# Kernel tuning notes

Measured on AMD Instinct MI355X. Metric: run time of the kernel, lower is better.

The kernel has to match this reference:

```python
import jax, jax.numpy as jnp
import numpy as np

N, H, I, B = 128, 128, 2, 8192

def _gru(x, h, Wih, Whh, bih, bhh):
    # torch.nn.GRUCell semantics; gates ordered (r, z, n)
    gi = x @ Wih.T + bih              # [B, 3H]
    gh = h @ Whh.T + bhh              # [B, 3H]
    ir, iz, ic = jnp.split(gi, 3, axis=1)
    hr, hz, hc = jnp.split(gh, 3, axis=1)
    r = jax.nn.sigmoid(ir + hr)
    z = jax.nn.sigmoid(iz + hz)
    n = jnp.tanh(ic + r * hc)
    return (1.0 - z) * n + z * h

def setup_inputs() -> dict:
    key = jax.random.key(0)
    ks = jax.random.split(key, 13)
    s = 0.1  # ~1/sqrt(H) init scale
    return {
        "inputs": jax.random.uniform(ks[0], (B, I), jnp.float32),
        "Wih0": jax.random.normal(ks[1], (N, 3 * H, I), jnp.float32) * s,
        "Whh0": jax.random.normal(ks[2], (N, 3 * H, H), jnp.float32) * s,
        "bih0": jax.random.normal(ks[3], (N, 3 * H), jnp.float32) * s,
        "bhh0": jax.random.normal(ks[4], (N, 3 * H), jnp.float32) * s,
        "Wih1": jax.random.normal(ks[5], (N, 3 * H, H), jnp.float32) * s,
        "Whh1": jax.random.normal(ks[6], (N, 3 * H, H), jnp.float32) * s,
        "bih1": jax.random.normal(ks[7], (N, 3 * H), jnp.float32) * s,
        "bhh1": jax.random.normal(ks[8], (N, 3 * H), jnp.float32) * s,
        "W1": jax.random.normal(ks[9], (N, H, H), jnp.float32) * s,
        "b1": jax.random.normal(ks[10], (N, H), jnp.float32) * s,
        "W2": jax.random.normal(ks[11], (N, I, H), jnp.float32) * s,
        "b2": jax.random.normal(ks[12], (N, I), jnp.float32) * s,
    }

def reference(inputs, Wih0, Whh0, bih0, bhh0, Wih1, Whh1, bih1, bhh1, W1, b1, W2, b2):
    batch = inputs.shape[0]
    h0 = jnp.zeros((batch, H), inputs.dtype)
    sample_keys = jax.random.split(jax.random.key(42), N)

    def step(carry, xs):
        inp, h1, h2 = carry
        (wih0, whh0, bi0, bh0, wih1, whh1, bi1, bh1, w1, bb1, w2, bb2, k) = xs
        h1 = _gru(inp, h1, wih0, whh0, bi0, bh0)
        h2 = _gru(h1, h2, wih1, whh1, bi1, bh1)
        s = jnp.cos(h2) + 1e-10
        hdn = jax.nn.relu(s @ w1.T + bb1)
        p = jax.nn.softmax(hdn @ w2.T + bb2, axis=1) + 1e-10  # probs + eps, as in torch
        sample = jax.lax.stop_gradient(jax.random.categorical(k, jnp.log(p)))
        nxt = jax.nn.one_hot(sample, I, dtype=p.dtype)
        return (nxt, h1, h2), p

    xs = (Wih0, Whh0, bih0, bhh0, Wih1, Whh1, bih1, bhh1, W1, b1, W2, b2, sample_keys)
    _, probs = jax.lax.scan(step, (inputs, h0, h0), xs)  # probs: [N, B, I]
    return jnp.transpose(probs, (1, 0, 2))  # [B, N, I]
```

## Files before the change

### kernel.cpp

```cpp
#include <hip/hip_runtime.h>
#include <cstdint>


namespace {

constexpr int NSTEPS = 128;
constexpr int HDIM = 128;
constexpr int G3H = 384;

constexpr int BTM = 32;
constexpr int THM = 512;
constexpr int S0P = 385;
constexpr int S1P = 513;

constexpr int BT = 16;
constexpr int THREADS = 256;
constexpr int HP = 132;
constexpr int SP = 516;

typedef _Float16 half8 __attribute__((ext_vector_type(8)));
typedef float f32x4 __attribute__((ext_vector_type(4)));

constexpr float LO_SCALE = 4096.0f;
constexpr float LO_INV = 2.44140625e-4f;
constexpr float F16_MIN_NORM = 6.104e-5f;
constexpr float LOG2E = 1.4426950408889634f;
constexpr float INV2PI = 0.15915494309189535f;

__device__ __forceinline__ void split_f16(float x, _Float16& a1, _Float16& a2s) {
  _Float16 h = (fabsf(x) < F16_MIN_NORM) ? (_Float16)0.0f : (_Float16)x;
  a1 = h;
  a2s = (_Float16)((x - (float)h) * LO_SCALE);
}

__device__ __forceinline__ void tf2x32(uint32_t k0, uint32_t k1,
                                       uint32_t x0, uint32_t x1,
                                       uint32_t& o0, uint32_t& o1) {
  const uint32_t ks2 = k0 ^ k1 ^ 0x1BD11BDAu;
  uint32_t v0 = x0 + k0;
  uint32_t v1 = x1 + k1;
  const uint32_t ks[3] = {k0, k1, ks2};
  const uint32_t rotA[4] = {13u, 15u, 26u, 6u};
  const uint32_t rotB[4] = {17u, 29u, 16u, 24u};
#pragma unroll
  for (int i = 0; i < 5; ++i) {
#pragma unroll
    for (int j = 0; j < 4; ++j) {
      const uint32_t r = (i & 1) ? rotB[j] : rotA[j];
      v0 += v1;
      v1 = (v1 << r) | (v1 >> (32u - r));
      v1 ^= v0;
    }
    v0 += ks[(i + 1) % 3];
    v1 += ks[(i + 2) % 3] + (uint32_t)(i + 1);
  }
  o0 = v0;
  o1 = v1;
}

__device__ __forceinline__ float u01_from_bits(uint32_t bits) {
  const float tiny = 1.1754943508222875e-38f;
  float f = __uint_as_float((bits >> 9) | 0x3F800000u) - 1.0f;
  float u = f * (1.0f - tiny) + tiny;
  return fmaxf(tiny, u);
}

__device__ __forceinline__ float fexp2(float x) { return __builtin_amdgcn_exp2f(x); }
__device__ __forceinline__ float frcp(float x) { return __builtin_amdgcn_rcpf(x); }
__device__ __forceinline__ float sigmoidf(float x) {
  return frcp(1.0f + fexp2(-LOG2E * x));
}
__device__ __forceinline__ float ftanhf(float x) {
  return 1.0f - 2.0f * frcp(1.0f + fexp2((2.0f * LOG2E) * x));
}
__device__ __forceinline__ float fcosx(float x) {
  return __builtin_amdgcn_cosf(x * INV2PI);
}

__device__ __forceinline__ float dot4(const float4 a, const float4 b, float c) {
  c = fmaf(a.x, b.x, c);
  c = fmaf(a.y, b.y, c);
  c = fmaf(a.z, b.z, c);
  c = fmaf(a.w, b.w, c);
  return c;
}

__device__ __forceinline__ void load_Afrag(const _Float16* arr, int lane,
                                           half8 (&A)[2][4]) {
#pragma unroll
  for (int mt = 0; mt < 2; ++mt)
#pragma unroll
    for (int kt = 0; kt < 4; ++kt)
      A[mt][kt] = *(const half8*)(arr + mt * 2048 + (kt * 64 + lane) * 8);
}

__device__ __forceinline__ void load_B(const _Float16* __restrict__ B1,
                                       const _Float16* __restrict__ B2,
                                       int jt, int lane,
                                       half8 (&b1)[4], half8 (&b2)[4]) {
#pragma unroll
  for (int kt = 0; kt < 4; ++kt) {
    const size_t o = ((size_t)(jt * 4 + kt) * 64 + lane) * 8;
    b1[kt] = *(const half8*)(B1 + o);
    b2[kt] = *(const half8*)(B2 + o);
  }
}

__device__ __forceinline__ void mfma_regs(const half8 (&A1)[2][4],
                                          const half8 (&A2)[2][4],
                                          const half8 (&b1)[4],
                                          const half8 (&b2)[4],
                                          f32x4 (&c1)[2], f32x4 (&c2)[2]) {
#pragma unroll
  for (int kt = 0; kt < 4; ++kt)
#pragma unroll
    for (int mt = 0; mt < 2; ++mt) {
      c1[mt] = __builtin_amdgcn_mfma_f32_16x16x32_f16(A1[mt][kt], b1[kt], c1[mt], 0, 0, 0);
      c2[mt] = __builtin_amdgcn_mfma_f32_16x16x32_f16(A1[mt][kt], b2[kt], c2[mt], 0, 0, 0);
      c2[mt] = __builtin_amdgcn_mfma_f32_16x16x32_f16(A2[mt][kt], b1[kt], c2[mt], 0, 0, 0);
    }
}

}

extern "C" __global__ __launch_bounds__(256)
void preprocess_split_kernel(const float* __restrict__ src,
                             _Float16* __restrict__ d1,
                             _Float16* __restrict__ d2,
                             int total, int JT) {
  const int idx = blockIdx.x * 256 + threadIdx.x;
  if (idx >= total) return;
  const int lane = idx & 63;
  const int kt = (idx >> 6) & 3;
  const int rest = idx >> 8;
  const int jt = rest % JT;
  const int nstep = rest / JT;

  const int j = jt * 16 + (lane & 15);
  const int k0 = kt * 32 + ((lane >> 4) << 3);
  const float* p = src + ((size_t)nstep * (JT * 16) + j) * 128 + k0;
  const float4 w0 = *(const float4*)p;
  const float4 w1 = *(const float4*)(p + 4);
  const float xs[8] = {w0.x, w0.y, w0.z, w0.w, w1.x, w1.y, w1.z, w1.w};

  half8 o1, o2;
#pragma unroll
  for (int t = 0; t < 8; ++t) {
    _Float16 a1, a2s;
    split_f16(xs[t], a1, a2s);
    o1[t] = a1;
    o2[t] = a2s;
  }
  *(half8*)(d1 + (size_t)idx * 8) = o1;
  *(half8*)(d2 + (size_t)idx * 8) = o2;
}

extern "C" __global__ __launch_bounds__(512, 2)
void rnn_wavefn_mfma_kernel(const float* __restrict__ inputs,
                            const float* __restrict__ Wih0,
                            const float* __restrict__ bih0,
                            const float* __restrict__ bhh0,
                            const float* __restrict__ bih1,
                            const float* __restrict__ bhh1,
                            const float* __restrict__ b1,
                            const float* __restrict__ W2,
                            const float* __restrict__ b2,
                            const _Float16* __restrict__ Whh0_1,
                            const _Float16* __restrict__ Whh0_2,
                            const _Float16* __restrict__ Wih1_1,
                            const _Float16* __restrict__ Wih1_2,
                            const _Float16* __restrict__ Whh1_1,
                            const _Float16* __restrict__ Whh1_2,
                            const _Float16* __restrict__ W1_1,
                            const _Float16* __restrict__ W1_2,
                            float* __restrict__ out) {
  __shared__ __align__(16) float S0[BTM][S0P];
  __shared__ float S1[BTM][S1P];
  __shared__ _Float16 h1A1[4096], h1A2[4096];
  __shared__ _Float16 h2A1[4096], h2A2[4096];
  __shared__ float xin[BTM][2];
  __shared__ uint32_t skey[NSTEPS][2];

  _Float16* const csA1 = (_Float16*)&S0[0][0];
  _Float16* const csA2 = csA1 + 4096;

  const int tid = threadIdx.x;
  const int b0 = blockIdx.x * BTM;
  const int wv = tid >> 6;
  const int lane = tid & 63;
  const int lm = lane & 15;
  const int m0 = (lane >> 4) * 4;

  const int cb = tid & 31;
  const int ct5 = tid >> 5;
  const int d0 = ct5 * 8;
  const int ibase = ((cb >> 4) * 2048 +
                     (((ct5 >> 2) << 6) + ((ct5 & 3) << 4) + (cb & 15)) * 8);

  float h1r[8], h2r[8];
#pragma unroll
  for (int i = 0; i < 8; ++i) { h1r[i] = 0.0f; h2r[i] = 0.0f; }
  for (int i = tid; i < 4096; i += THM) {
    h1A1[i] = (_Float16)0.0f; h1A2[i] = (_Float16)0.0f;
    h2A1[i] = (_Float16)0.0f; h2A2[i] = (_Float16)0.0f;
  }
  if (tid < BTM * 2) {
    xin[tid >> 1][tid & 1] = inputs[(b0 + (tid >> 1)) * 2 + (tid & 1)];
  }
  if (tid < NSTEPS) {
    uint32_t a, bk;
    tf2x32(0u, 42u, 0u, (uint32_t)tid, a, bk);
    skey[tid][0] = a;
    skey[tid][1] = bk;
  }
  __syncthreads();

  auto do_out = [&](int np) {
    const float* __restrict__ W2p = W2 + (size_t)np * 2 * HDIM;
    const float* __restrict__ b2p = b2 + (size_t)np * 2;
    const int ln = tid & 15;
    const int ob = tid >> 4;
    const int kb = ln * 8;
    float a0 = 0.0f, a1 = 0.0f;
#pragma unroll
    for (int k = 0; k < 8; ++k) {
      const float hd = S1[ob][384 + kb + k];
      a0 = fmaf(W2p[kb + k], hd, a0);
      a1 = fmaf(W2p[HDIM + kb + k], hd, a1);
    }
#pragma unroll
    for (int off = 8; off >= 1; off >>= 1) {
      a0 += __shfl_xor(a0, off, 16);
      a1 += __shfl_xor(a1, off, 16);
    }
    if (ln < 2) {
      const float l0 = a0 + b2p[0];
      const float l1 = a1 + b2p[1];
      const float m = fmaxf(l0, l1);
      const float e0 = expf(l0 - m);
      const float e1 = expf(l1 - m);
      const float sum = e0 + e1;
      const float p0 = e0 / sum + 1e-10f;
      const float p1 = e1 / sum + 1e-10f;
      const int gb = b0 + ob;
      uint32_t o0, o1;
      tf2x32(skey[np][0], skey[np][1], 0u, (uint32_t)(2 * gb + ln), o0, o1);
      const float u = u01_from_bits(o0 ^ o1);
      const float g = -logf(-logf(u));
      const float zv = logf((ln == 0) ? p0 : p1) + g;
      const float zo = __shfl_xor(zv, 1, 16);
      if (ln == 0) {
        out[((size_t)gb * NSTEPS + np) * 2 + 0] = p0;
        out[((size_t)gb * NSTEPS + np) * 2 + 1] = p1;
        const int smp = (zo > zv) ? 1 : 0;
        xin[ob][0] = (smp == 0) ? 1.0f : 0.0f;
        xin[ob][1] = (smp == 1) ? 1.0f : 0.0f;
      }
    }
  };

  half8 Bb1[2][4], Bb2[2][4];
  load_B(Whh0_1, Whh0_2, wv * 3, lane, Bb1[0], Bb2[0]);

  for (int n = 0; n < NSTEPS; ++n) {
    const float* __restrict__ Wih0n = Wih0 + (size_t)n * G3H * 2;
    const float* __restrict__ bih0n = bih0 + (size_t)n * G3H;
    const float* __restrict__ bhh0n = bhh0 + (size_t)n * G3H;
    const float* __restrict__ bih1n = bih1 + (size_t)n * G3H;
    const float* __restrict__ bhh1n = bhh1 + (size_t)n * G3H;
    const float* __restrict__ b1n = b1 + (size_t)n * HDIM;
    const size_t fo3 = (size_t)n * 49152;
    const size_t fo1 = (size_t)n * 16384;

    {
      half8 A1[2][4], A2[2][4];
      load_Afrag(h1A1, lane, A1);
      load_Afrag(h1A2, lane, A2);
      float bv[6];
#pragma unroll
      for (int t = 0; t < 6; ++t)
        bv[t] = ((t < 3) ? bhh0n : bhh1n)[(wv * 3 + (t % 3)) * 16 + lm];
#pragma unroll
      for (int t = 0; t < 6; ++t) {
        const int cur = t & 1;
        if (t < 5) {
          const int tn = t + 1;
          const _Float16* nB1 = (tn < 3) ? (Whh0_1 + fo3) : (Whh1_1 + fo3);
          const _Float16* nB2 = (tn < 3) ? (Whh0_2 + fo3) : (Whh1_2 + fo3);
          load_B(nB1, nB2, wv * 3 + (tn % 3), lane, Bb1[cur ^ 1], Bb2[cur ^ 1]);
        }
        if (t == 3) {
          load_Afrag(h2A1, lane, A1);
          load_Afrag(h2A2, lane, A2);
        }
        const int jt = wv * 3 + (t % 3);
        f32x4 c1[2] = {{0.f,0.f,0.f,0.f},{0.f,0.f,0.f,0.f}};
        f32x4 c2[2] = {{0.f,0.f,0.f,0.f},{0.f,0.f,0.f,0.f}};
        mfma_regs(A1, A2, Bb1[cur], Bb2[cur], c1, c2);
        const int col = jt * 16 + lm;
        if (t < 3) {
#pragma unroll
          for (int mt = 0; mt < 2; ++mt)
#pragma unroll
            for (int r = 0; r < 4; ++r)
              S0[mt * 16 + m0 + r][col] = bv[t] + fmaf(c2[mt][r], LO_INV, c1[mt][r]);
        } else {
#pragma unroll
          for (int mt = 0; mt < 2; ++mt)
#pragma unroll
            for (int r = 0; r < 4; ++r)
              S1[mt * 16 + m0 + r][col] = bv[t] + fmaf(c2[mt][r], LO_INV, c1[mt][r]);
        }
      }
    }
    if (n > 0) do_out(n - 1);
    __syncthreads();

    {
      load_B(Wih1_1 + fo3, Wih1_2 + fo3, wv * 3, lane, Bb1[0], Bb2[0]);
      const float x0 = xin[cb][0];
      const float x1 = xin[cb][1];
      float wr[16], wz[16], wn[16], br[8], bz[8], bn[8];
#pragma unroll
      for (int q = 0; q < 4; ++q) {
        *(float4*)&wr[q * 4] = *(const float4*)(Wih0n + d0 * 2 + q * 4);
        *(float4*)&wz[q * 4] = *(const float4*)(Wih0n + (d0 + 128) * 2 + q * 4);
        *(float4*)&wn[q * 4] = *(const float4*)(Wih0n + (d0 + 256) * 2 + q * 4);
      }
      *(float4*)&br[0] = *(const float4*)(bih0n + d0);
      *(float4*)&br[4] = *(const float4*)(bih0n + d0 + 4);
      *(float4*)&bz[0] = *(const float4*)(bih0n + 128 + d0);
      *(float4*)&bz[4] = *(const float4*)(bih0n + 128 + d0 + 4);
      *(float4*)&bn[0] = *(const float4*)(bih0n + 256 + d0);
      *(float4*)&bn[4] = *(const float4*)(bih0n + 256 + d0 + 4);
      half8 o1, o2;
#pragma unroll
      for (int j = 0; j < 8; ++j) {
        const int d = d0 + j;
        const float gir = fmaf(wr[2 * j], x0, fmaf(wr[2 * j + 1], x1, br[j]));
        const float giz = fmaf(wz[2 * j], x0, fmaf(wz[2 * j + 1], x1, bz[j]));
        const float gin = fmaf(wn[2 * j], x0, fmaf(wn[2 * j + 1], x1, bn[j]));
        const float r = sigmoidf(gir + S0[cb][d]);
        const float z = sigmoidf(giz + S0[cb][d + 128]);
        const float nn = ftanhf(gin + r * S0[cb][d + 256]);
        const float h1n = (1.0f - z) * nn + z * h1r[j];
        h1r[j] = h1n;
        _Float16 a1, a2s;
        split_f16(h1n, a1, a2s);
        o1[j] = a1;
        o2[j] = a2s;
      }
      *(half8*)(h1A1 + ibase) = o1;
      *(half8*)(h1A2 + ibase) = o2;
    }
    __syncthreads();

    {
      half8 A1[2][4], A2[2][4];
      load_Afrag(h1A1, lane, A1);
      load_Afrag(h1A2, lane, A2);
      float bv[3];
#pragma unroll
      for (int t = 0; t < 3; ++t) bv[t] = bih1n[(wv * 3 + t) * 16 + lm];
#pragma unroll
      for (int t = 0; t < 3; ++t) {
        const int cur = t & 1;
        if (t < 2)
          load_B(Wih1_1 + fo3, Wih1_2 + fo3, wv * 3 + t + 1, lane,
                 Bb1[cur ^ 1], Bb2[cur ^ 1]);
        const int jt = wv * 3 + t;
        f32x4 c1[2] = {{0.f,0.f,0.f,0.f},{0.f,0.f,0.f,0.f}};
        f32x4 c2[2] = {{0.f,0.f,0.f,0.f},{0.f,0.f,0.f,0.f}};
        mfma_regs(A1, A2, Bb1[cur], Bb2[cur], c1, c2);
        const int col = jt * 16 + lm;
        if (jt < 16) {
#pragma unroll
          for (int mt = 0; mt < 2; ++mt)
#pragma unroll
            for (int r = 0; r < 4; ++r)
              S1[mt * 16 + m0 + r][col] += bv[t] + fmaf(c2[mt][r], LO_INV, c1[mt][r]);
        } else {
#pragma unroll
          for (int mt = 0; mt < 2; ++mt)
#pragma unroll
            for (int r = 0; r < 4; ++r)
              S1[mt * 16 + m0 + r][col + 128] = bv[t] + fmaf(c2[mt][r], LO_INV, c1[mt][r]);
        }
      }
    }
    __syncthreads();

    half8 hb1[4], hb2[4];
    {
      load_B(W1_1 + fo1, W1_2 + fo1, wv, lane, hb1, hb2);
      const size_t fo3n = (size_t)((n + 1 < NSTEPS) ? n + 1 : n) * 49152;
      load_B(Whh0_1 + fo3n, Whh0_2 + fo3n, wv * 3, lane, Bb1[0], Bb2[0]);
      half8 o1, o2, p1, p2;
#pragma unroll
      for (int j = 0; j < 8; ++j) {
        const int d = d0 + j;
        const float r = sigmoidf(S1[cb][d]);
        const float z = sigmoidf(S1[cb][d + 128]);
        const float nn = ftanhf(S1[cb][d + 384] + r * S1[cb][d + 256]);
        const float h2n = (1.0f - z) * nn + z * h2r[j];
        h2r[j] = h2n;
        _Float16 a1, a2s;
        split_f16(h2n, a1, a2s);
        o1[j] = a1;
        o2[j] = a2s;
        const float cv = fcosx(h2n) + 1e-10f;
        split_f16(cv, a1, a2s);
        p1[j] = a1;
        p2[j] = a2s;
      }
      *(half8*)(h2A1 + ibase) = o1;
      *(half8*)(h2A2 + ibase) = o2;
      *(half8*)(csA1 + ibase) = p1;
      *(half8*)(csA2 + ibase) = p2;
    }
    __syncthreads();

    {
      const float bias = b1n[wv * 16 + lm];
      half8 A1[2][4], A2[2][4];
      load_Afrag(csA1, lane, A1);
      load_Afrag(csA2, lane, A2);
      f32x4 c1[2] = {{0.f,0.f,0.f,0.f},{0.f,0.f,0.f,0.f}};
      f32x4 c2[2] = {{0.f,0.f,0.f,0.f},{0.f,0.f,0.f,0.f}};
      mfma_regs(A1, A2, hb1, hb2, c1, c2);
      const int col = wv * 16 + lm;
#pragma unroll
      for (int mt = 0; mt < 2; ++mt)
#pragma unroll
        for (int r = 0; r < 4; ++r)
          S1[mt * 16 + m0 + r][384 + col] =
              fmaxf(bias + fmaf(c2[mt][r], LO_INV, c1[mt][r]), 0.0f);
    }
    __syncthreads();
  }

  do_out(NSTEPS - 1);
}

extern "C" __global__ __launch_bounds__(256, 2)
void rnn_wavefn_fp32_kernel(const float* __restrict__ inputs,
                            const float* __restrict__ Wih0,
                            const float* __restrict__ Whh0,
                            const float* __restrict__ bih0,
                            const float* __restrict__ bhh0,
                            const float* __restrict__ Wih1,
                            const float* __restrict__ Whh1,
                            const float* __restrict__ bih1,
                            const float* __restrict__ bhh1,
                            const float* __restrict__ W1,
                            const float* __restrict__ b1,
                            const float* __restrict__ W2,
                            const float* __restrict__ b2,
                            float* __restrict__ out) {
  __shared__ float h1[BT][HP];
  __shared__ float h2[BT][HP];
  __shared__ float S[BT][SP];
  __shared__ float xin[BT][2];

  const int tid = threadIdx.x;
  const int b0 = blockIdx.x * BT;
  const int tj = tid >> 2;
  const int tq = tid & 3;

  for (int i = tid; i < BT * HP; i += THREADS) {
    ((float*)h1)[i] = 0.0f;
    ((float*)h2)[i] = 0.0f;
  }
  if (tid < BT * 2) {
    xin[tid >> 1][tid & 1] = inputs[(b0 + (tid >> 1)) * 2 + (tid & 1)];
  }
  __syncthreads();

  for (int n = 0; n < NSTEPS; ++n) {
    const float* __restrict__ Wih0n = Wih0 + (size_t)n * G3H * 2;
    const float* __restrict__ Whh0n = Whh0 + (size_t)n * G3H * HDIM;
    const float* __restrict__ bih0n = bih0 + (size_t)n * G3H;
    const float* __restrict__ bhh0n = bhh0 + (size_t)n * G3H;
    const float* __restrict__ Wih1n = Wih1 + (size_t)n * G3H * HDIM;
    const float* __restrict__ Whh1n = Whh1 + (size_t)n * G3H * HDIM;
    const float* __restrict__ bih1n = bih1 + (size_t)n * G3H;
    const float* __restrict__ bhh1n = bhh1 + (size_t)n * G3H;
    const float* __restrict__ W1n = W1 + (size_t)n * HDIM * HDIM;
    const float* __restrict__ b1n = b1 + (size_t)n * HDIM;
    const float* __restrict__ W2n = W2 + (size_t)n * 2 * HDIM;
    const float* __restrict__ b2n = b2 + (size_t)n * 2;

    {
      float acc[6][4];
#pragma unroll
      for (int g = 0; g < 6; ++g) {
        const float bias = bhh0n[tj + g * 64];
#pragma unroll
        for (int i = 0; i < 4; ++i) acc[g][i] = bias;
      }
      for (int kk = 0; kk < HDIM; kk += 16) {
#pragma unroll
        for (int s = 0; s < 4; ++s) {
          const int k = kk + s * 4;
          float4 w[6];
#pragma unroll
          for (int g = 0; g < 6; ++g)
            w[g] = *(const float4*)(Whh0n + (size_t)(tj + g * 64) * HDIM + k);
#pragma unroll
          for (int i = 0; i < 4; ++i) {
            const float4 hv = *(const float4*)&h1[tq + 4 * i][k];
#pragma unroll
            for (int g = 0; g < 6; ++g) acc[g][i] = dot4(w[g], hv, acc[g][i]);
          }
        }
      }
#pragma unroll
      for (int g = 0; g < 6; ++g)
#pragma unroll
        for (int i = 0; i < 4; ++i) S[tq + 4 * i][tj + g * 64] = acc[g][i];
    }
    __syncthreads();

#pragma unroll
    for (int rep = 0; rep < (BT * HDIM) / THREADS; ++rep) {
      const int idx = tid + rep * THREADS;
      const int b = idx >> 7;
      const int d = idx & 127;
      const float x0 = xin[b][0];
      const float x1 = xin[b][1];
      const float gir = fmaf(Wih0n[d * 2 + 0], x0, fmaf(Wih0n[d * 2 + 1], x1, bih0n[d]));
      const float giz = fmaf(Wih0n[(d + 128) * 2 + 0], x0,
                             fmaf(Wih0n[(d + 128) * 2 + 1], x1, bih0n[d + 128]));
      const float gin = fmaf(Wih0n[(d + 256) * 2 + 0], x0,
                             fmaf(Wih0n[(d + 256) * 2 + 1], x1, bih0n[d + 256]));
      const float r = sigmoidf(gir + S[b][d]);
      const float z = sigmoidf(giz + S[b][d + 128]);
      const float nn = tanhf(gin + r * S[b][d + 256]);
      h1[b][d] = (1.0f - z) * nn + z * h1[b][d];
    }
    __syncthreads();

    {
      float acc[6][4];
#pragma unroll
      for (int g = 0; g < 6; ++g) {
        const float bias = bhh1n[tj + g * 64];
#pragma unroll
        for (int i = 0; i < 4; ++i) acc[g][i] = bias;
      }
      for (int kk = 0; kk < HDIM; kk += 16) {
#pragma unroll
        for (int s = 0; s < 4; ++s) {
          const int k = kk + s * 4;
          float4 w[6];
#pragma unroll
          for (int g = 0; g < 6; ++g)
            w[g] = *(const float4*)(Whh1n + (size_t)(tj + g * 64) * HDIM + k);
#pragma unroll
          for (int i = 0; i < 4; ++i) {
            const float4 hv = *(const float4*)&h2[tq + 4 * i][k];
#pragma unroll
            for (int g = 0; g < 6; ++g) acc[g][i] = dot4(w[g], hv, acc[g][i]);
          }
        }
      }
#pragma unroll
      for (int g = 0; g < 6; ++g)
#pragma unroll
        for (int i = 0; i < 4; ++i) S[tq + 4 * i][tj + g * 64] = acc[g][i];
    }

    {
      float acc[6][4];
#pragma unroll
      for (int g = 0; g < 6; ++g) {
        const float bias = bih1n[tj + g * 64];
#pragma unroll
        for (int i = 0; i < 4; ++i) acc[g][i] = bias;
      }
      for (int kk = 0; kk < HDIM; kk += 16) {
#pragma unroll
        for (int s = 0; s < 4; ++s) {
          const int k = kk + s * 4;
          float4 w[6];
#pragma unroll
          for (int g = 0; g < 6; ++g)
            w[g] = *(const float4*)(Wih1n + (size_t)(tj + g * 64) * HDIM + k);
#pragma unroll
          for (int i = 0; i < 4; ++i) {
            const float4 hv = *(const float4*)&h1[tq + 4 * i][k];
#pragma unroll
            for (int g = 0; g < 6; ++g) acc[g][i] = dot4(w[g], hv, acc[g][i]);
          }
        }
      }
#pragma unroll
      for (int g = 0; g < 6; ++g) {
        const int row = tj + g * 64;
#pragma unroll
        for (int i = 0; i < 4; ++i) {
          if (row < 256) S[tq + 4 * i][row] += acc[g][i];
          else           S[tq + 4 * i][row + 128] = acc[g][i];
        }
      }
    }
    __syncthreads();

#pragma unroll
    for (int rep = 0; rep < (BT * HDIM) / THREADS; ++rep) {
      const int idx = tid + rep * THREADS;
      const int b = idx >> 7;
      const int d = idx & 127;
      const float r = sigmoidf(S[b][d]);
      const float z = sigmoidf(S[b][d + 128]);
      const float nn = tanhf(S[b][d + 384] + r * S[b][d + 256]);
      const float h2n = (1.0f - z) * nn + z * h2[b][d];
      h2[b][d] = h2n;
      S[b][d] = cosf(h2n) + 1e-10f;
    }
    __syncthreads();

    {
      float acc[2][4];
#pragma unroll
      for (int g = 0; g < 2; ++g) {
        const float bias = b1n[tj + g * 64];
#pragma unroll
        for (int i = 0; i < 4; ++i) acc[g][i] = bias;
      }
      for (int kk = 0; kk < HDIM; kk += 16) {
#pragma unroll
        for (int s = 0; s < 4; ++s) {
          const int k = kk + s * 4;
          float4 w[2];
          w[0] = *(const float4*)(W1n + (size_t)(tj)*HDIM + k);
          w[1] = *(const float4*)(W1n + (size_t)(tj + 64) * HDIM + k);
#pragma unroll
          for (int i = 0; i < 4; ++i) {
            const float4 sv = *(const float4*)&S[tq + 4 * i][k];
            acc[0][i] = dot4(w[0], sv, acc[0][i]);
            acc[1][i] = dot4(w[1], sv, acc[1][i]);
          }
        }
      }
#pragma unroll
      for (int g = 0; g < 2; ++g)
#pragma unroll
        for (int i = 0; i < 4; ++i)
          S[tq + 4 * i][384 + tj + g * 64] = fmaxf(acc[g][i], 0.0f);
    }
    __syncthreads();

    {
      const int ln = tid & 15;
      const int b = tid >> 4;
      const int kb = ln * 8;
      float a0 = 0.0f, a1 = 0.0f;
#pragma unroll
      for (int k = 0; k < 8; ++k) {
        const float hd = S[b][384 + kb + k];
        a0 = fmaf(W2n[kb + k], hd, a0);
        a1 = fmaf(W2n[HDIM + kb + k], hd, a1);
      }
#pragma unroll
      for (int off = 8; off >= 1; off >>= 1) {
        a0 += __shfl_xor(a0, off, 16);
        a1 += __shfl_xor(a1, off, 16);
      }
      if (ln == 0) {
        const float l0 = a0 + b2n[0];
        const float l1 = a1 + b2n[1];
        const float m = fmaxf(l0, l1);
        const float e0 = expf(l0 - m);
        const float e1 = expf(l1 - m);
        const float sum = e0 + e1;
        const float p0 = e0 / sum + 1e-10f;
        const float p1 = e1 / sum + 1e-10f;
        const int gb = b0 + b;
        out[((size_t)gb * NSTEPS + n) * 2 + 0] = p0;
        out[((size_t)gb * NSTEPS + n) * 2 + 1] = p1;

        uint32_t k0n, k1n;
        tf2x32(0u, 42u, 0u, (uint32_t)n, k0n, k1n);
        uint32_t o0, o1;
        tf2x32(k0n, k1n, 0u, (uint32_t)(2 * gb), o0, o1);
        const float u0 = u01_from_bits(o0 ^ o1);
        tf2x32(k0n, k1n, 0u, (uint32_t)(2 * gb + 1), o0, o1);
        const float u1 = u01_from_bits(o0 ^ o1);
        const float g0 = -logf(-logf(u0));
        const float g1 = -logf(-logf(u1));
        const float z0 = logf(p0) + g0;
        const float z1 = logf(p1) + g1;
        const int smp = (z1 > z0) ? 1 : 0;
        xin[b][0] = (smp == 0) ? 1.0f : 0.0f;
        xin[b][1] = (smp == 1) ? 1.0f : 0.0f;
      }
    }
    __syncthreads();
  }
}

extern "C" void kernel_launch(void* const* d_in, const int* in_sizes, int n_in,
                              void* d_out, int out_size, void* d_ws, size_t ws_size,
                              hipStream_t stream) {
  (void)in_sizes; (void)n_in; (void)out_size;
  const float* inputs = (const float*)d_in[0];
  const float* Wih0 = (const float*)d_in[1];
  const float* Whh0 = (const float*)d_in[2];
  const float* bih0 = (const float*)d_in[3];
  const float* bhh0 = (const float*)d_in[4];
  const float* Wih1 = (const float*)d_in[5];
  const float* Whh1 = (const float*)d_in[6];
  const float* bih1 = (const float*)d_in[7];
  const float* bhh1 = (const float*)d_in[8];
  const float* W1 = (const float*)d_in[9];
  const float* b1 = (const float*)d_in[10];
  const float* W2 = (const float*)d_in[11];
  const float* b2 = (const float*)d_in[12];
  float* out = (float*)d_out;

  constexpr size_t EB = 6291456;
  constexpr size_t EW1 = 2097152;
  constexpr size_t WS_NEEDED = (6 * EB + 2 * EW1) * sizeof(_Float16);

  if (ws_size >= WS_NEEDED) {
    _Float16* w = (_Float16*)d_ws;
    _Float16* Whh0_1 = w;
    _Float16* Whh0_2 = w + EB;
    _Float16* Wih1_1 = w + 2 * EB;
    _Float16* Wih1_2 = w + 3 * EB;
    _Float16* Whh1_1 = w + 4 * EB;
    _Float16* Whh1_2 = w + 5 * EB;
    _Float16* W1_1 = w + 6 * EB;
    _Float16* W1_2 = w + 6 * EB + EW1;

    hipLaunchKernelGGL(preprocess_split_kernel, dim3(3072), dim3(256), 0, stream,
                       Whh0, Whh0_1, Whh0_2, 786432, 24);
    hipLaunchKernelGGL(preprocess_split_kernel, dim3(3072), dim3(256), 0, stream,
                       Wih1, Wih1_1, Wih1_2, 786432, 24);
    hipLaunchKernelGGL(preprocess_split_kernel, dim3(3072), dim3(256), 0, stream,
                       Whh1, Whh1_1, Whh1_2, 786432, 24);
    hipLaunchKernelGGL(preprocess_split_kernel, dim3(1024), dim3(256), 0, stream,
                       W1, W1_1, W1_2, 262144, 8);
    hipLaunchKernelGGL(rnn_wavefn_mfma_kernel, dim3(8192 / BTM), dim3(THM), 0, stream,
                       inputs, Wih0, bih0, bhh0, bih1, bhh1, b1, W2, b2,
                       Whh0_1, Whh0_2, Wih1_1, Wih1_2, Whh1_1, Whh1_2, W1_1, W1_2,
                       out);
  } else {
    hipLaunchKernelGGL(rnn_wavefn_fp32_kernel, dim3(8192 / BT), dim3(THREADS), 0, stream,
                       inputs, Wih0, Whh0, bih0, bhh0, Wih1, Whh1, bih1, bhh1,
                       W1, b1, W2, b2, out);
  }
}
```

Before: 1.577 ms.

## Halve batch tile per block to 16 rows for more blocks

```diff
diff --git a/kernel.cpp b/kernel.cpp
--- a/kernel.cpp
+++ b/kernel.cpp
@@ -8,7 +8,7 @@
 constexpr int HDIM = 128;
 constexpr int G3H = 384;
 
-constexpr int BTM = 32;
+constexpr int BTM = 16;
 constexpr int THM = 512;
 constexpr int S0P = 385;
 constexpr int S1P = 513;
@@ -19,6 +19,7 @@
 constexpr int SP = 516;
 
 typedef _Float16 half8 __attribute__((ext_vector_type(8)));
+typedef _Float16 half4 __attribute__((ext_vector_type(4)));
 typedef float f32x4 __attribute__((ext_vector_type(4)));
 
 constexpr float LO_SCALE = 4096.0f;
@@ -85,13 +86,11 @@
   return c;
 }
 
-__device__ __forceinline__ void load_Afrag(const _Float16* arr, int lane,
-                                           half8 (&A)[2][4]) {
-#pragma unroll
-  for (int mt = 0; mt < 2; ++mt)
-#pragma unroll
-    for (int kt = 0; kt < 4; ++kt)
-      A[mt][kt] = *(const half8*)(arr + mt * 2048 + (kt * 64 + lane) * 8);
+__device__ __forceinline__ void load_Afrag1(const _Float16* arr, int lane,
+                                            half8 (&A)[4]) {
+#pragma unroll
+  for (int kt = 0; kt < 4; ++kt)
+    A[kt] = *(const half8*)(arr + (kt * 64 + lane) * 8);
 }
 
 __device__ __forceinline__ void load_B(const _Float16* __restrict__ B1,
@@ -106,19 +105,17 @@
   }
 }
 
-__device__ __forceinline__ void mfma_regs(const half8 (&A1)[2][4],
-                                          const half8 (&A2)[2][4],
-                                          const half8 (&b1)[4],
-                                          const half8 (&b2)[4],
-                                          f32x4 (&c1)[2], f32x4 (&c2)[2]) {
-#pragma unroll
-  for (int kt = 0; kt < 4; ++kt)
-#pragma unroll
-    for (int mt = 0; mt < 2; ++mt) {
-      c1[mt] = __builtin_amdgcn_mfma_f32_16x16x32_f16(A1[mt][kt], b1[kt], c1[mt], 0, 0, 0);
-      c2[mt] = __builtin_amdgcn_mfma_f32_16x16x32_f16(A1[mt][kt], b2[kt], c2[mt], 0, 0, 0);
-      c2[mt] = __builtin_amdgcn_mfma_f32_16x16x32_f16(A2[mt][kt], b1[kt], c2[mt], 0, 0, 0);
-    }
+__device__ __forceinline__ void mfma_regs1(const half8 (&A1)[4],
+                                           const half8 (&A2)[4],
+                                           const half8 (&b1)[4],
+                                           const half8 (&b2)[4],
+                                           f32x4& c1, f32x4& c2) {
+#pragma unroll
+  for (int kt = 0; kt < 4; ++kt) {
+    c1 = __builtin_amdgcn_mfma_f32_16x16x32_f16(A1[kt], b1[kt], c1, 0, 0, 0);
+    c2 = __builtin_amdgcn_mfma_f32_16x16x32_f16(A1[kt], b2[kt], c2, 0, 0, 0);
+    c2 = __builtin_amdgcn_mfma_f32_16x16x32_f16(A2[kt], b1[kt], c2, 0, 0, 0);
+  }
 }
 
 }
@@ -176,13 +173,13 @@
                             float* __restrict__ out) {
   __shared__ __align__(16) float S0[BTM][S0P];
   __shared__ float S1[BTM][S1P];
-  __shared__ _Float16 h1A1[4096], h1A2[4096];
-  __shared__ _Float16 h2A1[4096], h2A2[4096];
+  __shared__ _Float16 h1A1[2048], h1A2[2048];
+  __shared__ _Float16 h2A1[2048], h2A2[2048];
   __shared__ float xin[BTM][2];
   __shared__ uint32_t skey[NSTEPS][2];
 
   _Float16* const csA1 = (_Float16*)&S0[0][0];
-  _Float16* const csA2 = csA1 + 4096;
+  _Float16* const csA2 = csA1 + 2048;
 
   const int tid = threadIdx.x;
   const int b0 = blockIdx.x * BTM;
@@ -191,16 +188,16 @@
   const int lm = lane & 15;
   const int m0 = (lane >> 4) * 4;
 
-  const int cb = tid & 31;
-  const int ct5 = tid >> 5;
-  const int d0 = ct5 * 8;
-  const int ibase = ((cb >> 4) * 2048 +
-                     (((ct5 >> 2) << 6) + ((ct5 & 3) << 4) + (cb & 15)) * 8);
-
-  float h1r[8], h2r[8];
-#pragma unroll
-  for (int i = 0; i < 8; ++i) { h1r[i] = 0.0f; h2r[i] = 0.0f; }
-  for (int i = tid; i < 4096; i += THM) {
+  const int cb = tid & 15;
+  const int ct5 = tid >> 4;
+  const int d0 = ct5 * 4;
+  const int ibase4 = ((ct5 >> 3) * 64 + ((ct5 >> 1) & 3) * 16 + cb) * 8 +
+                     (ct5 & 1) * 4;
+
+  float h1r[4], h2r[4];
+#pragma unroll
+  for (int i = 0; i < 4; ++i) { h1r[i] = 0.0f; h2r[i] = 0.0f; }
+  for (int i = tid; i < 2048; i += THM) {
     h1A1[i] = (_Float16)0.0f; h1A2[i] = (_Float16)0.0f;
     h2A1[i] = (_Float16)0.0f; h2A2[i] = (_Float16)0.0f;
   }
@@ -220,41 +217,43 @@
     const float* __restrict__ b2p = b2 + (size_t)np * 2;
     const int ln = tid & 15;
     const int ob = tid >> 4;
-    const int kb = ln * 8;
-    float a0 = 0.0f, a1 = 0.0f;
-#pragma unroll
-    for (int k = 0; k < 8; ++k) {
-      const float hd = S1[ob][384 + kb + k];
-      a0 = fmaf(W2p[kb + k], hd, a0);
-      a1 = fmaf(W2p[HDIM + kb + k], hd, a1);
-    }
-#pragma unroll
-    for (int off = 8; off >= 1; off >>= 1) {
-      a0 += __shfl_xor(a0, off, 16);
-      a1 += __shfl_xor(a1, off, 16);
-    }
-    if (ln < 2) {
-      const float l0 = a0 + b2p[0];
-      const float l1 = a1 + b2p[1];
-      const float m = fmaxf(l0, l1);
-      const float e0 = expf(l0 - m);
-      const float e1 = expf(l1 - m);
-      const float sum = e0 + e1;
-      const float p0 = e0 / sum + 1e-10f;
-      const float p1 = e1 / sum + 1e-10f;
-      const int gb = b0 + ob;
-      uint32_t o0, o1;
-      tf2x32(skey[np][0], skey[np][1], 0u, (uint32_t)(2 * gb + ln), o0, o1);
-      const float u = u01_from_bits(o0 ^ o1);
-      const float g = -logf(-logf(u));
-      const float zv = logf((ln == 0) ? p0 : p1) + g;
-      const float zo = __shfl_xor(zv, 1, 16);
-      if (ln == 0) {
-        out[((size_t)gb * NSTEPS + np) * 2 + 0] = p0;
-        out[((size_t)gb * NSTEPS + np) * 2 + 1] = p1;
-        const int smp = (zo > zv) ? 1 : 0;
-        xin[ob][0] = (smp == 0) ? 1.0f : 0.0f;
-        xin[ob][1] = (smp == 1) ? 1.0f : 0.0f;
+    if (ob < BTM) {
+      const int kb = ln * 8;
+      float a0 = 0.0f, a1 = 0.0f;
+#pragma unroll
+      for (int k = 0; k < 8; ++k) {
+        const float hd = S1[ob][384 + kb + k];
+        a0 = fmaf(W2p[kb + k], hd, a0);
+        a1 = fmaf(W2p[HDIM + kb + k], hd, a1);
+      }
+#pragma unroll
+      for (int off = 8; off >= 1; off >>= 1) {
+        a0 += __shfl_xor(a0, off, 16);
+        a1 += __shfl_xor(a1, off, 16);
+      }
+      if (ln < 2) {
+        const float l0 = a0 + b2p[0];
+        const float l1 = a1 + b2p[1];
+        const float m = fmaxf(l0, l1);
+        const float e0 = expf(l0 - m);
+        const float e1 = expf(l1 - m);
+        const float sum = e0 + e1;
+        const float p0 = e0 / sum + 1e-10f;
+        const float p1 = e1 / sum + 1e-10f;
+        const int gb = b0 + ob;
+        uint32_t o0, o1;
+        tf2x32(skey[np][0], skey[np][1], 0u, (uint32_t)(2 * gb + ln), o0, o1);
+        const float u = u01_from_bits(o0 ^ o1);
+        const float g = -logf(-logf(u));
+        const float zv = logf((ln == 0) ? p0 : p1) + g;
+        const float zo = __shfl_xor(zv, 1, 16);
+        if (ln == 0) {
+          out[((size_t)gb * NSTEPS + np) * 2 + 0] = p0;
+          out[((size_t)gb * NSTEPS + np) * 2 + 1] = p1;
+          const int smp = (zo > zv) ? 1 : 0;
+          xin[ob][0] = (smp == 0) ? 1.0f : 0.0f;
+          xin[ob][1] = (smp == 1) ? 1.0f : 0.0f;
+        }
       }
     }
   };
@@ -273,9 +272,9 @@
     const size_t fo1 = (size_t)n * 16384;
 
     {
-      half8 A1[2][4], A2[2][4];
-      load_Afrag(h1A1, lane, A1);
-      load_Afrag(h1A2, lane, A2);
+      half8 A1[4], A2[4];
+      load_Afrag1(h1A1, lane, A1);
+      load_Afrag1(h1A2, lane, A2);
       float bv[6];
 #pragma unroll
       for (int t = 0; t < 6; ++t)
@@ -290,26 +289,22 @@
           load_B(nB1, nB2, wv * 3 + (tn % 3), lane, Bb1[cur ^ 1], Bb2[cur ^ 1]);
         }
         if (t == 3) {
-          load_Afrag(h2A1, lane, A1);
-          load_Afrag(h2A2, lane, A2);
+          load_Afrag1(h2A1, lane, A1);
+          load_Afrag1(h2A2, lane, A2);
         }
         const int jt = wv * 3 + (t % 3);
-        f32x4 c1[2] = {{0.f,0.f,0.f,0.f},{0.f,0.f,0.f,0.f}};
-        f32x4 c2[2] = {{0.f,0.f,0.f,0.f},{0.f,0.f,0.f,0.f}};
-        mfma_regs(A1, A2, Bb1[cur], Bb2[cur], c1, c2);
+        f32x4 c1 = {0.f, 0.f, 0.f, 0.f};
+        f32x4 c2 = {0.f, 0.f, 0.f, 0.f};
+        mfma_regs1(A1, A2, Bb1[cur], Bb2[cur], c1, c2);
         const int col = jt * 16 + lm;
         if (t < 3) {
 #pragma unroll
-          for (int mt = 0; mt < 2; ++mt)
-#pragma unroll
-            for (int r = 0; r < 4; ++r)
-              S0[mt * 16 + m0 + r][col] = bv[t] + fmaf(c2[mt][r], LO_INV, c1[mt][r]);
+          for (int r = 0; r < 4; ++r)
+            S0[m0 + r][col] = bv[t] + fmaf(c2[r], LO_INV, c1[r]);
         } else {
 #pragma unroll
-          for (int mt = 0; mt < 2; ++mt)
-#pragma unroll
-            for (int r = 0; r < 4; ++r)
-              S1[mt * 16 + m0 + r][col] = bv[t] + fmaf(c2[mt][r], LO_INV, c1[mt][r]);
+          for (int r = 0; r < 4; ++r)
+            S1[m0 + r][col] = bv[t] + fmaf(c2[r], LO_INV, c1[r]);
         }
       }
     }
@@ -320,22 +315,19 @@
       load_B(Wih1_1 + fo3, Wih1_2 + fo3, wv * 3, lane, Bb1[0], Bb2[0]);
       const float x0 = xin[cb][0];
       const float x1 = xin[cb][1];
-      float wr[16], wz[16], wn[16], br[8], bz[8], bn[8];
-#pragma unroll
-      for (int q = 0; q < 4; ++q) {
+      float wr[8], wz[8], wn[8], br[4], bz[4], bn[4];
+#pragma unroll
+      for (int q = 0; q < 2; ++q) {
         *(float4*)&wr[q * 4] = *(const float4*)(Wih0n + d0 * 2 + q * 4);
         *(float4*)&wz[q * 4] = *(const float4*)(Wih0n + (d0 + 128) * 2 + q * 4);
         *(float4*)&wn[q * 4] = *(const float4*)(Wih0n + (d0 + 256) * 2 + q * 4);
       }
       *(float4*)&br[0] = *(const float4*)(bih0n + d0);
-      *(float4*)&br[4] = *(const float4*)(bih0n + d0 + 4);
       *(float4*)&bz[0] = *(const float4*)(bih0n + 128 + d0);
-      *(float4*)&bz[4] = *(const float4*)(bih0n + 128 + d0 + 4);
       *(float4*)&bn[0] = *(const float4*)(bih0n + 256 + d0);
-      *(float4*)&bn[4] = *(const float4*)(bih0n + 256 + d0 + 4);
-      half8 o1, o2;
-#pragma unroll
-      for (int j = 0; j < 8; ++j) {
+      half4 o1, o2;
+#pragma unroll
+      for (int j = 0; j < 4; ++j) {
         const int d = d0 + j;
         const float gir = fmaf(wr[2 * j], x0, fmaf(wr[2 * j + 1], x1, br[j]));
         const float giz = fmaf(wz[2 * j], x0, fmaf(wz[2 * j + 1], x1, bz[j]));
@@ -350,15 +342,15 @@
         o1[j] = a1;
         o2[j] = a2s;
       }
-      *(half8*)(h1A1 + ibase) = o1;
-      *(half8*)(h1A2 + ibase) = o2;
-    }
-    __syncthreads();
-
-    {
-      half8 A1[2][4], A2[2][4];
-      load_Afrag(h1A1, lane, A1);
-      load_Afrag(h1A2, lane, A2);
+      *(half4*)(h1A1 + ibase4) = o1;
+      *(half4*)(h1A2 + ibase4) = o2;
+    }
+    __syncthreads();
+
+    {
+      half8 A1[4], A2[4];
+      load_Afrag1(h1A1, lane, A1);
+      load_Afrag1(h1A2, lane, A2);
       float bv[3];
 #pragma unroll
       for (int t = 0; t < 3; ++t) bv[t] = bih1n[(wv * 3 + t) * 16 + lm];
@@ -369,22 +361,18 @@
           load_B(Wih1_1 + fo3, Wih1_2 + fo3, wv * 3 + t + 1, lane,
                  Bb1[cur ^ 1], Bb2[cur ^ 1]);
         const int jt = wv * 3 + t;
-        f32x4 c1[2] = {{0.f,0.f,0.f,0.f},{0.f,0.f,0.f,0.f}};
-        f32x4 c2[2] = {{0.f,0.f,0.f,0.f},{0.f,0.f,0.f,0.f}};
-        mfma_regs(A1, A2, Bb1[cur], Bb2[cur], c1, c2);
+        f32x4 c1 = {0.f, 0.f, 0.f, 0.f};
+        f32x4 c2 = {0.f, 0.f, 0.f, 0.f};
+        mfma_regs1(A1, A2, Bb1[cur], Bb2[cur], c1, c2);
         const int col = jt * 16 + lm;
         if (jt < 16) {
 #pragma unroll
-          for (int mt = 0; mt < 2; ++mt)
-#pragma unroll
-            for (int r = 0; r < 4; ++r)
-              S1[mt * 16 + m0 + r][col] += bv[t] + fmaf(c2[mt][r], LO_INV, c1[mt][r]);
+          for (int r = 0; r < 4; ++r)
+            S1[m0 + r][col] += bv[t] + fmaf(c2[r], LO_INV, c1[r]);
         } else {
 #pragma unroll
-          for (int mt = 0; mt < 2; ++mt)
-#pragma unroll
-            for (int r = 0; r < 4; ++r)
-              S1[mt * 16 + m0 + r][col + 128] = bv[t] + fmaf(c2[mt][r], LO_INV, c1[mt][r]);
+          for (int r = 0; r < 4; ++r)
+            S1[m0 + r][col + 128] = bv[t] + fmaf(c2[r], LO_INV, c1[r]);
         }
       }
     }
@@ -395,9 +383,9 @@
       load_B(W1_1 + fo1, W1_2 + fo1, wv, lane, hb1, hb2);
       const size_t fo3n = (size_t)((n + 1 < NSTEPS) ? n + 1 : n) * 49152;
       load_B(Whh0_1 + fo3n, Whh0_2 + fo3n, wv * 3, lane, Bb1[0], Bb2[0]);
-      half8 o1, o2, p1, p2;
-#pragma unroll
-      for (int j = 0; j < 8; ++j) {
+      half4 o1, o2, p1, p2;
+#pragma unroll
+      for (int j = 0; j < 4; ++j) {
         const int d = d0 + j;
         const float r = sigmoidf(S1[cb][d]);
         const float z = sigmoidf(S1[cb][d + 128]);
@@ -413,28 +401,26 @@
         p1[j] = a1;
         p2[j] = a2s;
       }
-      *(half8*)(h2A1 + ibase) = o1;
-      *(half8*)(h2A2 + ibase) = o2;
-      *(half8*)(csA1 + ibase) = p1;
-      *(half8*)(csA2 + ibase) = p2;
+      *(half4*)(h2A1 + ibase4) = o1;
+      *(half4*)(h2A2 + ibase4) = o2;
+      *(half4*)(csA1 + ibase4) = p1;
+      *(half4*)(csA2 + ibase4) = p2;
     }
     __syncthreads();
 
     {
       const float bias = b1n[wv * 16 + lm];
-      half8 A1[2][4], A2[2][4];
-      load_Afrag(csA1, lane, A1);
-      load_Afrag(csA2, lane, A2);
-      f32x4 c1[2] = {{0.f,0.f,0.f,0.f},{0.f,0.f,0.f,0.f}};
-      f32x4 c2[2] = {{0.f,0.f,0.f,0.f},{0.f,0.f,0.f,0.f}};
-      mfma_regs(A1, A2, hb1, hb2, c1, c2);
+      half8 A1[4], A2[4];
+      load_Afrag1(csA1, lane, A1);
+      load_Afrag1(csA2, lane, A2);
+      f32x4 c1 = {0.f, 0.f, 0.f, 0.f};
+      f32x4 c2 = {0.f, 0.f, 0.f, 0.f};
+      mfma_regs1(A1, A2, hb1, hb2, c1, c2);
       const int col = wv * 16 + lm;
 #pragma unroll
-      for (int mt = 0; mt < 2; ++mt)
-#pragma unroll
-        for (int r = 0; r < 4; ++r)
-          S1[mt * 16 + m0 + r][384 + col] =
-              fmaxf(bias + fmaf(c2[mt][r], LO_INV, c1[mt][r]), 0.0f);
+      for (int r = 0; r < 4; ++r)
+        S1[m0 + r][384 + col] =
+            fmaxf(bias + fmaf(c2[r], LO_INV, c1[r]), 0.0f);
     }
     __syncthreads();
   }
```

Result: slower. 2.520 ms (+59.7%).

## Keep layer-0 GRU hidden gates in registers and double-buffer h1 fragments

Applied to the files above, without the earlier changes.

```diff
diff --git a/kernel.cpp b/kernel.cpp
--- a/kernel.cpp
+++ b/kernel.cpp
@@ -10,7 +10,6 @@
 
 constexpr int BTM = 32;
 constexpr int THM = 512;
-constexpr int S0P = 385;
 constexpr int S1P = 513;
 
 constexpr int BT = 16;
@@ -174,15 +173,12 @@
                             const _Float16* __restrict__ W1_1,
                             const _Float16* __restrict__ W1_2,
                             float* __restrict__ out) {
-  __shared__ __align__(16) float S0[BTM][S0P];
   __shared__ float S1[BTM][S1P];
-  __shared__ _Float16 h1A1[4096], h1A2[4096];
+  __shared__ _Float16 h1A1[2][4096], h1A2[2][4096];
   __shared__ _Float16 h2A1[4096], h2A2[4096];
+  __shared__ _Float16 csA1[4096], csA2[4096];
   __shared__ float xin[BTM][2];
   __shared__ uint32_t skey[NSTEPS][2];
-
-  _Float16* const csA1 = (_Float16*)&S0[0][0];
-  _Float16* const csA2 = csA1 + 4096;
 
   const int tid = threadIdx.x;
   const int b0 = blockIdx.x * BTM;
@@ -191,17 +187,24 @@
   const int lm = lane & 15;
   const int m0 = (lane >> 4) * 4;
 
+  const int dcol = wv * 16 + lm;
+  const int kt_ = wv >> 1;
+  const int hi_ = ((wv & 1) << 1) + (lm >> 3);
+  const int j_ = lm & 7;
+
   const int cb = tid & 31;
   const int ct5 = tid >> 5;
   const int d0 = ct5 * 8;
   const int ibase = ((cb >> 4) * 2048 +
                      (((ct5 >> 2) << 6) + ((ct5 & 3) << 4) + (cb & 15)) * 8);
 
-  float h1r[8], h2r[8];
-#pragma unroll
-  for (int i = 0; i < 8; ++i) { h1r[i] = 0.0f; h2r[i] = 0.0f; }
+  float h1C[8];
+  float h2r[8];
+#pragma unroll
+  for (int i = 0; i < 8; ++i) { h1C[i] = 0.0f; h2r[i] = 0.0f; }
   for (int i = tid; i < 4096; i += THM) {
-    h1A1[i] = (_Float16)0.0f; h1A2[i] = (_Float16)0.0f;
+    h1A1[0][i] = (_Float16)0.0f; h1A1[1][i] = (_Float16)0.0f;
+    h1A2[0][i] = (_Float16)0.0f; h1A2[1][i] = (_Float16)0.0f;
     h2A1[i] = (_Float16)0.0f; h2A2[i] = (_Float16)0.0f;
   }
   if (tid < BTM * 2) {
@@ -260,7 +263,9 @@
   };
 
   half8 Bb1[2][4], Bb2[2][4];
-  load_B(Whh0_1, Whh0_2, wv * 3, lane, Bb1[0], Bb2[0]);
+  load_B(Whh0_1, Whh0_2, wv, lane, Bb1[0], Bb2[0]);
+
+  float g_r[2][4], g_z[2][4], g_n[2][4];
 
   for (int n = 0; n < NSTEPS; ++n) {
     const float* __restrict__ Wih0n = Wih0 + (size_t)n * G3H * 2;
@@ -271,94 +276,98 @@
     const float* __restrict__ b1n = b1 + (size_t)n * HDIM;
     const size_t fo3 = (size_t)n * 49152;
     const size_t fo1 = (size_t)n * 16384;
+    const int p = n & 1;
 
     {
       half8 A1[2][4], A2[2][4];
-      load_Afrag(h1A1, lane, A1);
-      load_Afrag(h1A2, lane, A2);
-      float bv[6];
-#pragma unroll
-      for (int t = 0; t < 6; ++t)
-        bv[t] = ((t < 3) ? bhh0n : bhh1n)[(wv * 3 + (t % 3)) * 16 + lm];
-#pragma unroll
-      for (int t = 0; t < 6; ++t) {
+      load_Afrag(h1A1[p ^ 1], lane, A1);
+      load_Afrag(h1A2[p ^ 1], lane, A2);
+      const float bvr = bhh0n[dcol];
+      const float bvz = bhh0n[dcol + 128];
+      const float bvn = bhh0n[dcol + 256];
+#pragma unroll
+      for (int t = 0; t < 3; ++t) {
         const int cur = t & 1;
-        if (t < 5) {
-          const int tn = t + 1;
-          const _Float16* nB1 = (tn < 3) ? (Whh0_1 + fo3) : (Whh1_1 + fo3);
-          const _Float16* nB2 = (tn < 3) ? (Whh0_2 + fo3) : (Whh1_2 + fo3);
-          load_B(nB1, nB2, wv * 3 + (tn % 3), lane, Bb1[cur ^ 1], Bb2[cur ^ 1]);
-        }
-        if (t == 3) {
-          load_Afrag(h2A1, lane, A1);
-          load_Afrag(h2A2, lane, A2);
-        }
-        const int jt = wv * 3 + (t % 3);
+        if (t < 2)
+          load_B(Whh0_1 + fo3, Whh0_2 + fo3, wv + 8 * (t + 1), lane,
+                 Bb1[cur ^ 1], Bb2[cur ^ 1]);
         f32x4 c1[2] = {{0.f,0.f,0.f,0.f},{0.f,0.f,0.f,0.f}};
         f32x4 c2[2] = {{0.f,0.f,0.f,0.f},{0.f,0.f,0.f,0.f}};
         mfma_regs(A1, A2, Bb1[cur], Bb2[cur], c1, c2);
-        const int col = jt * 16 + lm;
-        if (t < 3) {
-#pragma unroll
-          for (int mt = 0; mt < 2; ++mt)
-#pragma unroll
-            for (int r = 0; r < 4; ++r)
-              S0[mt * 16 + m0 + r][col] = bv[t] + fmaf(c2[mt][r], LO_INV, c1[mt][r]);
-        } else {
-#pragma unroll
-          for (int mt = 0; mt < 2; ++mt)
-#pragma unroll
-            for (int r = 0; r < 4; ++r)
-              S1[mt * 16 + m0 + r][col] = bv[t] + fmaf(c2[mt][r], LO_INV, c1[mt][r]);
+        const float bias = (t == 0) ? bvr : (t == 1) ? bvz : bvn;
+#pragma unroll
+        for (int mt = 0; mt < 2; ++mt)
+#pragma unroll
+          for (int r = 0; r < 4; ++r) {
+            const float v = bias + fmaf(c2[mt][r], LO_INV, c1[mt][r]);
+            if (t == 0)      g_r[mt][r] = v;
+            else if (t == 1) g_z[mt][r] = v;
+            else             g_n[mt][r] = v;
+          }
+      }
+    }
+    if (n > 0) do_out(n - 1);
+    __syncthreads();
+
+    {
+      load_B(Whh1_1 + fo3, Whh1_2 + fo3, wv * 3, lane, Bb1[0], Bb2[0]);
+      const float2 wr2 = *(const float2*)(Wih0n + dcol * 2);
+      const float2 wz2 = *(const float2*)(Wih0n + (dcol + 128) * 2);
+      const float2 wn2 = *(const float2*)(Wih0n + (dcol + 256) * 2);
+      const float br = bih0n[dcol];
+      const float bz = bih0n[dcol + 128];
+      const float bn = bih0n[dcol + 256];
+#pragma unroll
+      for (int mt = 0; mt < 2; ++mt)
+#pragma unroll
+        for (int r = 0; r < 4; ++r) {
+          const int b = mt * 16 + m0 + r;
+          const float x0 = xin[b][0];
+          const float x1 = xin[b][1];
+          const float gir = fmaf(wr2.x, x0, fmaf(wr2.y, x1, br));
+          const float giz = fmaf(wz2.x, x0, fmaf(wz2.y, x1, bz));
+          const float gin = fmaf(wn2.x, x0, fmaf(wn2.y, x1, bn));
+          const float rr = sigmoidf(gir + g_r[mt][r]);
+          const float zz = sigmoidf(giz + g_z[mt][r]);
+          const float nn = ftanhf(gin + rr * g_n[mt][r]);
+          const float h1n = (1.0f - zz) * nn + zz * h1C[mt * 4 + r];
+          h1C[mt * 4 + r] = h1n;
+          _Float16 a1h, a2h;
+          split_f16(h1n, a1h, a2h);
+          const int ao = mt * 2048 + (kt_ * 64 + hi_ * 16 + (m0 + r)) * 8 + j_;
+          h1A1[p][ao] = a1h;
+          h1A2[p][ao] = a2h;
         }
-      }
-    }
-    if (n > 0) do_out(n - 1);
-    __syncthreads();
-
-    {
+      half8 A1[2][4], A2[2][4];
+      load_Afrag(h2A1, lane, A1);
+      load_Afrag(h2A2, lane, A2);
+      float bv[3];
+#pragma unroll
+      for (int t = 0; t < 3; ++t) bv[t] = bhh1n[(wv * 3 + t) * 16 + lm];
+#pragma unroll
+      for (int t = 0; t < 3; ++t) {
+        const int cur = t & 1;
+        if (t < 2)
+          load_B(Whh1_1 + fo3, Whh1_2 + fo3, wv * 3 + t + 1, lane,
+                 Bb1[cur ^ 1], Bb2[cur ^ 1]);
+        f32x4 c1[2] = {{0.f,0.f,0.f,0.f},{0.f,0.f,0.f,0.f}};
+        f32x4 c2[2] = {{0.f,0.f,0.f,0.f},{0.f,0.f,0.f,0.f}};
+        mfma_regs(A1, A2, Bb1[cur], Bb2[cur], c1, c2);
+        const int col = (wv * 3 + t) * 16 + lm;
+#pragma unroll
+        for (int mt = 0; mt < 2; ++mt)
+#pragma unroll
+          for (int r = 0; r < 4; ++r)
+            S1[mt * 16 + m0 + r][col] = bv[t] + fmaf(c2[mt][r], LO_INV, c1[mt][r]);
+      }
       load_B(Wih1_1 + fo3, Wih1_2 + fo3, wv * 3, lane, Bb1[0], Bb2[0]);
-      const float x0 = xin[cb][0];
-      const float x1 = xin[cb][1];
-      float wr[16], wz[16], wn[16], br[8], bz[8], bn[8];
-#pragma unroll
-      for (int q = 0; q < 4; ++q) {
-        *(float4*)&wr[q * 4] = *(const float4*)(Wih0n + d0 * 2 + q * 4);
-        *(float4*)&wz[q * 4] = *(const float4*)(Wih0n + (d0 + 128) * 2 + q * 4);
-        *(float4*)&wn[q * 4] = *(const float4*)(Wih0n + (d0 + 256) * 2 + q * 4);
-      }
-      *(float4*)&br[0] = *(const float4*)(bih0n + d0);
-      *(float4*)&br[4] = *(const float4*)(bih0n + d0 + 4);
-      *(float4*)&bz[0] = *(const float4*)(bih0n + 128 + d0);
-      *(float4*)&bz[4] = *(const float4*)(bih0n + 128 + d0 + 4);
-      *(float4*)&bn[0] = *(const float4*)(bih0n + 256 + d0);
-      *(float4*)&bn[4] = *(const float4*)(bih0n + 256 + d0 + 4);
-      half8 o1, o2;
-#pragma unroll
-      for (int j = 0; j < 8; ++j) {
-        const int d = d0 + j;
-        const float gir = fmaf(wr[2 * j], x0, fmaf(wr[2 * j + 1], x1, br[j]));
-        const float giz = fmaf(wz[2 * j], x0, fmaf(wz[2 * j + 1], x1, bz[j]));
-        const float gin = fmaf(wn[2 * j], x0, fmaf(wn[2 * j + 1], x1, bn[j]));
-        const float r = sigmoidf(gir + S0[cb][d]);
-        const float z = sigmoidf(giz + S0[cb][d + 128]);
-        const float nn = ftanhf(gin + r * S0[cb][d + 256]);
-        const float h1n = (1.0f - z) * nn + z * h1r[j];
-        h1r[j] = h1n;
-        _Float16 a1, a2s;
-        split_f16(h1n, a1, a2s);
-        o1[j] = a1;
-        o2[j] = a2s;
-      }
-      *(half8*)(h1A1 + ibase) = o1;
-      *(half8*)(h1A2 + ibase) = o2;
     }
     __syncthreads();
 
     {
       half8 A1[2][4], A2[2][4];
-      load_Afrag(h1A1, lane, A1);
-      load_Afrag(h1A2, lane, A2);
+      load_Afrag(h1A1[p], lane, A1);
+      load_Afrag(h1A2[p], lane, A2);
       float bv[3];
 #pragma unroll
       for (int t = 0; t < 3; ++t) bv[t] = bih1n[(wv * 3 + t) * 16 + lm];
@@ -394,7 +403,7 @@
     {
       load_B(W1_1 + fo1, W1_2 + fo1, wv, lane, hb1, hb2);
       const size_t fo3n = (size_t)((n + 1 < NSTEPS) ? n + 1 : n) * 49152;
-      load_B(Whh0_1 + fo3n, Whh0_2 + fo3n, wv * 3, lane, Bb1[0], Bb2[0]);
+      load_B(Whh0_1 + fo3n, Whh0_2 + fo3n, wv, lane, Bb1[0], Bb2[0]);
       half8 o1, o2, p1, p2;
 #pragma unroll
       for (int j = 0; j < 8; ++j) {
```

Result: slower. 2.194 ms (+39.1%).
